# Kernel optimization log

Hardware: AMD Instinct MI355X
Metric: run time of the kernel (lower is better)

The kernel has to match this reference:

```python
import jax, jax.numpy as jnp
import numpy as np

N = 100_000   # nodes
E = 1_600_000 # edges
NEG_SLOPE = 0.2

def _glorot(key, shape):
    fan = shape[0] + shape[-1]
    return jax.random.uniform(key, shape, jnp.float32, -1.0, 1.0) * np.sqrt(6.0 / fan)

def setup_inputs() -> dict:
    key = jax.random.key(0)
    ks = jax.random.split(key, 16)
    x = jax.random.normal(ks[0], (N, 2), jnp.float32)
    edge_index = jax.random.randint(ks[1], (2, E), 0, N)
    edge_weights = jax.random.uniform(ks[2], (E,), jnp.float32)
    # GATConv 1: in=2, out=32, heads=4, edge_dim=1 (lin/lin_edge have no bias in PyG)
    W1    = _glorot(ks[3], (2, 128))
    We1   = _glorot(ks[4], (1, 128))
    attS1 = _glorot(ks[5], (4, 32))
    attD1 = _glorot(ks[6], (4, 32))
    attE1 = _glorot(ks[7], (4, 32))
    b1    = jnp.zeros((128,), jnp.float32)
    # GATConv 2: in=128, out=1, heads=1, concat=False
    W2    = _glorot(ks[8], (128, 1))
    We2   = _glorot(ks[9], (1, 1))
    attS2 = _glorot(ks[10], (1, 1))
    attD2 = _glorot(ks[11], (1, 1))
    attE2 = _glorot(ks[12], (1, 1))
    b2    = jnp.zeros((1,), jnp.float32)
    return dict(x=x, edge_index=edge_index, edge_weights=edge_weights,
                W1=W1, attS1=attS1, attD1=attD1, We1=We1, attE1=attE1, b1=b1,
                W2=W2, attS2=attS2, attD2=attD2, We2=We2, attE2=attE2, b2=b2)

def _gat_layer(x, src, dst, eattr, W, We, a_s, a_d, a_e, b, heads, outc, concat):
    n = x.shape[0]
    # add self-loops; fill_value='mean' -> self-loop edge_attr = mean of incoming edge attrs
    cnt = jax.ops.segment_sum(jnp.ones((eattr.shape[0],), eattr.dtype), dst, num_segments=n)
    loop_attr = jax.ops.segment_sum(eattr, dst, num_segments=n) / jnp.maximum(cnt, 1.0)[:, None]
    loop = jnp.arange(n, dtype=src.dtype)
    src = jnp.concatenate([src, loop])
    dst = jnp.concatenate([dst, loop])
    ea = jnp.concatenate([eattr, loop_attr], axis=0)          # [E+N, edge_dim]
    h = (x @ W).reshape(n, heads, outc)                        # [N,H,C]
    a_src = jnp.sum(h * a_s, axis=-1)                          # [N,H]
    a_dst = jnp.sum(h * a_d, axis=-1)                          # [N,H]
    a_edge = jnp.sum((ea @ We).reshape(-1, heads, outc) * a_e, axis=-1)  # [E+N,H]
    logits = jax.nn.leaky_relu(a_src[src] + a_dst[dst] + a_edge, NEG_SLOPE)
    # scatter-softmax grouped by destination node
    m = jax.ops.segment_max(logits, dst, num_segments=n)       # every node has a self-loop
    p = jnp.exp(logits - m[dst])
    s = jax.ops.segment_sum(p, dst, num_segments=n)
    alpha = p / (s[dst] + 1e-16)                               # [E+N,H]
    out = jax.ops.segment_sum(h[src] * alpha[..., None], dst, num_segments=n)  # [N,H,C]
    out = out.reshape(n, heads * outc) if concat else out.mean(axis=1)
    return out + b

def reference(x, edge_index, edge_weights, W1, attS1, attD1, We1, attE1, b1,
              W2, attS2, attD2, We2, attE2, b2):
    src, dst = edge_index[0], edge_index[1]
    ea = edge_weights[:, None]  # edge_dim=1
    h = _gat_layer(x, src, dst, ea, W1, We1, attS1, attD1, attE1, b1, 4, 32, True)
    h = jax.nn.elu(h)
    out = _gat_layer(h, src, dst, ea, W2, We2, attS2, attD2, attE2, b2, 1, 1, False)
    return out.squeeze(-1)  # [N]
```

## Files before the change

kernel.cpp:

```cpp
#include <hip/hip_runtime.h>

#define N_NODES 100000
#define N_EDGES 1600000
#define NQUAD (N_EDGES / 4)
#define NEG_SLOPE 0.2f

#define NBKT 512
#define BDIV 196
#define NUSED 511
#define PB 500
#define QPB (NQUAD / PB)
#define PBS 512
#define BCAP 4096

typedef int   vint4   __attribute__((ext_vector_type(4)));
typedef float vfloat4 __attribute__((ext_vector_type(4)));

__device__ __forceinline__ float leaky(float v) { return v >= 0.f ? v : NEG_SLOPE * v; }

__global__ void __launch_bounds__(256) k_hist(const int* __restrict__ ei,
                                              int* __restrict__ histT) {
    __shared__ int hist[NBKT];
    int tid = threadIdx.x;
    hist[tid] = 0;
    hist[tid + 256] = 0;
    __syncthreads();
    const vint4* dst4 = (const vint4*)(ei + N_EDGES);
    int q0 = blockIdx.x * QPB;
    for (int q = tid; q < QPB; q += 256) {
        vint4 d = __builtin_nontemporal_load(&dst4[q0 + q]);
        atomicAdd(&hist[d.x / BDIV], 1);
        atomicAdd(&hist[d.y / BDIV], 1);
        atomicAdd(&hist[d.z / BDIV], 1);
        atomicAdd(&hist[d.w / BDIV], 1);
    }
    __syncthreads();
    histT[tid * PBS + blockIdx.x] = hist[tid];
    histT[(tid + 256) * PBS + blockIdx.x] = hist[tid + 256];
}

__global__ void __launch_bounds__(512) k_rowscan(const int* __restrict__ histT,
                                                 int* __restrict__ offT,
                                                 int* __restrict__ btot) {
    __shared__ int sm[512];
    int b = blockIdx.x, tid = threadIdx.x;
    int v = (tid < PB) ? histT[b * PBS + tid] : 0;
    sm[tid] = v;
    __syncthreads();
    for (int off = 1; off < 512; off <<= 1) {
        int t = (tid >= off) ? sm[tid - off] : 0;
        __syncthreads();
        sm[tid] += t;
        __syncthreads();
    }
    if (tid < PB) offT[b * PBS + tid] = sm[tid] - v;
    if (tid == 511) btot[b] = sm[511];
}

__global__ void __launch_bounds__(512) k_bprefix(const int* __restrict__ btot,
                                                 int* __restrict__ bbase,
                                                 int* __restrict__ bcnt,
                                                 const float* __restrict__ W1,
                                                 const float* __restrict__ attS1,
                                                 const float* __restrict__ attD1,
                                                 const float* __restrict__ We1,
                                                 const float* __restrict__ attE1,
                                                 float* __restrict__ consts) {
    __shared__ int sm[512];
    int tid = threadIdx.x;
    if (tid < 8) {
        int r = tid >> 2, h = tid & 3;
        float s = 0.f;
        for (int c = 0; c < 32; ++c) s += W1[r * 128 + h * 32 + c] * attS1[h * 32 + c];
        consts[tid] = s;
    } else if (tid < 16) {
        int u = tid - 8, r = u >> 2, h = u & 3;
        float s = 0.f;
        for (int c = 0; c < 32; ++c) s += W1[r * 128 + h * 32 + c] * attD1[h * 32 + c];
        consts[tid] = s;
    } else if (tid < 20) {
        int h = tid - 16;
        float s = 0.f;
        for (int c = 0; c < 32; ++c) s += We1[h * 32 + c] * attE1[h * 32 + c];
        consts[tid] = s;
    }
    int v = btot[tid];
    sm[tid] = v;
    __syncthreads();
    for (int off = 1; off < 512; off <<= 1) {
        int t = (tid >= off) ? sm[tid - off] : 0;
        __syncthreads();
        sm[tid] += t;
        __syncthreads();
    }
    bbase[tid] = sm[tid] - v;
    bcnt[tid] = v;
}

__global__ void __launch_bounds__(512) k_part(const int* __restrict__ ei,
                                              const float* __restrict__ w,
                                              const int* __restrict__ offT,
                                              const int* __restrict__ bbase,
                                              const float* __restrict__ x,
                                              vint4* __restrict__ staging) {
    __shared__ int lcur[NBKT];
    int tid = threadIdx.x;
    lcur[tid] = offT[tid * PBS + blockIdx.x] + bbase[tid];
    __syncthreads();
    const vint4* src4 = (const vint4*)ei;
    const vint4* dst4 = (const vint4*)(ei + N_EDGES);
    const vfloat4* w4 = (const vfloat4*)w;
    int q0 = blockIdx.x * QPB;
    for (int q = tid; q < QPB; q += 512) {
        vint4 s = __builtin_nontemporal_load(&src4[q0 + q]);
        vint4 d = __builtin_nontemporal_load(&dst4[q0 + q]);
        vfloat4 ww = __builtin_nontemporal_load(&w4[q0 + q]);
#pragma unroll
        for (int j = 0; j < 4; ++j) {
            int dd = (j == 0) ? d.x : (j == 1) ? d.y : (j == 2) ? d.z : d.w;
            int ss = (j == 0) ? s.x : (j == 1) ? s.y : (j == 2) ? s.z : s.w;
            float wv = (j == 0) ? ww.x : (j == 1) ? ww.y : (j == 2) ? ww.z : ww.w;
            int b = dd / BDIV;
            int pos = atomicAdd(&lcur[b], 1);
            float2 xs = *(const float2*)(x + 2 * ss);
            vint4 r = {ss | ((dd - b * BDIV) << 17), __float_as_int(wv),
                       __float_as_int(xs.x), __float_as_int(xs.y)};
            staging[pos] = r;
        }
    }
}

__global__ void __launch_bounds__(512) k_bg1(const int* __restrict__ bbase,
                                             const int* __restrict__ bcnt,
                                             const vint4* __restrict__ staging,
                                             int2* __restrict__ csr2,
                                             const float* __restrict__ x,
                                             const float* __restrict__ consts,
                                             const float* __restrict__ W1,
                                             const float* __restrict__ b1,
                                             const float* __restrict__ W2,
                                             int* __restrict__ deg,
                                             int* __restrict__ rowst,
                                             float* __restrict__ h2,
                                             float* __restrict__ la) {
    __shared__ vint4 seg[BCAP];
    __shared__ float sw[BCAP], sx0[BCAP], sx1[BCAP];
    __shared__ int hist[256];
    __shared__ int lcur[BDIV], rowloc[BDIV], degL[BDIV];
    __shared__ float w10[132], w11[132], b1s[132], w2s[132];
    int b = blockIdx.x, tid = threadIdx.x;
    int base = bbase[b];
    int cnt = min(bcnt[b], BCAP);
    if (tid < 256) hist[tid] = 0;
    for (int j = tid; j < 128; j += 512) {
        int jj = (j >> 5) * 33 + (j & 31);
        w10[jj] = W1[j]; w11[jj] = W1[128 + j]; b1s[jj] = b1[j]; w2s[jj] = W2[j];
    }
    __syncthreads();
    for (int i = tid; i < cnt; i += 512) {
        vint4 r = staging[base + i];
        seg[i] = r;
        atomicAdd(&hist[r.x >> 17], 1);
    }
    __syncthreads();
    int v = (tid < 256) ? hist[tid] : 0;
    for (int off = 1; off < 256; off <<= 1) {
        int t = (tid < 256 && tid >= off) ? hist[tid - off] : 0;
        __syncthreads();
        if (tid < 256) hist[tid] += t;
        __syncthreads();
    }
    int n0 = b * BDIV;
    int nnode = min(BDIV, N_NODES - n0);
    if (tid < nnode) {
        deg[n0 + tid] = v;
        rowst[n0 + tid] = base + hist[tid] - v;
        degL[tid] = v;
        rowloc[tid] = hist[tid] - v;
        lcur[tid] = hist[tid] - v;
    }
    __syncthreads();
    for (int i = tid; i < cnt; i += 512) {
        vint4 r = seg[i];
        int dl = r.x >> 17;
        int pos = atomicAdd(&lcur[dl], 1);
        sw[pos] = __int_as_float(r.y);
        sx0[pos] = __int_as_float(r.z);
        sx1[pos] = __int_as_float(r.w);
        csr2[base + pos] = make_int2(r.x & 0x1FFFF, r.y);
    }
    __syncthreads();
    float c[20];
#pragma unroll
    for (int i = 0; i < 20; ++i) c[i] = consts[i];
    int g = tid >> 3, l = tid & 7;
    for (int j = g; j < nnode; j += 64) {
        int n = n0 + j;
        int rsL = rowloc[j], d = degL[j];
        float2 xn = *(const float2*)(x + 2 * n);
        float adv[4];
#pragma unroll
        for (int h = 0; h < 4; ++h) adv[h] = xn.x * c[8 + h] + xn.y * c[12 + h];
        float s[4] = {0, 0, 0, 0}, X0[4] = {0, 0, 0, 0}, X1[4] = {0, 0, 0, 0};
        float wsum = 0.f;
        for (int k = rsL + l; k < rsL + d; k += 8) {
            float wt = sw[k], x0s = sx0[k], x1s = sx1[k];
            wsum += wt;
#pragma unroll
            for (int h = 0; h < 4; ++h) {
                float as = x0s * c[h] + x1s * c[4 + h];
                float p = __expf(leaky(as + adv[h] + wt * c[16 + h]));
                s[h] += p;
                X0[h] += p * x0s;
                X1[h] += p * x1s;
            }
        }
#pragma unroll
        for (int off = 1; off < 8; off <<= 1) {
            wsum += __shfl_xor(wsum, off);
#pragma unroll
            for (int h = 0; h < 4; ++h) {
                s[h]  += __shfl_xor(s[h], off);
                X0[h] += __shfl_xor(X0[h], off);
                X1[h] += __shfl_xor(X1[h], off);
            }
        }
        float lav = wsum / fmaxf((float)d, 1.f);
#pragma unroll
        for (int h = 0; h < 4; ++h) {
            float aso = xn.x * c[h] + xn.y * c[4 + h];
            float p = __expf(leaky(aso + adv[h] + lav * c[16 + h]));
            s[h] += p;
            X0[h] += p * xn.x;
            X1[h] += p * xn.y;
        }
        int hh = l & 3;
        float sh  = (hh == 0) ? s[0]  : (hh == 1) ? s[1]  : (hh == 2) ? s[2]  : s[3];
        float X0h = (hh == 0) ? X0[0] : (hh == 1) ? X0[1] : (hh == 2) ? X0[2] : X0[3];
        float X1h = (hh == 0) ? X1[0] : (hh == 1) ? X1[1] : (hh == 2) ? X1[2] : X1[3];
        float inv = 1.f / (sh + 1e-16f);
        X0h *= inv;
        X1h *= inv;
        float acc = 0.f;
        int basej = hh * 33 + (l >> 2) * 16;
        for (int cc = 0; cc < 16; ++cc) {
            float vv = X0h * w10[basej + cc] + X1h * w11[basej + cc] + b1s[basej + cc];
            float el = vv > 0.f ? vv : __expf(vv) - 1.f;
            acc += el * w2s[basej + cc];
        }
        acc += __shfl_xor(acc, 1);
        acc += __shfl_xor(acc, 2);
        acc += __shfl_xor(acc, 4);
        if (l == 0) {
            h2[n] = acc;
            la[n] = lav;
        }
    }
}

__global__ void __launch_bounds__(256) k_gather2(const int* __restrict__ deg,
                                                 const int* __restrict__ rowst,
                                                 const int2* __restrict__ csr2,
                                                 const float* __restrict__ h2,
                                                 const float* __restrict__ la,
                                                 const float* __restrict__ attS2,
                                                 const float* __restrict__ attD2,
                                                 const float* __restrict__ We2,
                                                 const float* __restrict__ attE2,
                                                 const float* __restrict__ b2,
                                                 float* __restrict__ out) {
    int t = blockIdx.x * blockDim.x + threadIdx.x;
    int n = t >> 3, l = t & 7;
    if (n >= N_NODES) return;
    float aS = attS2[0], aD = attD2[0], cE = We2[0] * attE2[0], bb = b2[0];
    int rs = rowst[n], d = deg[n];
    float hn = h2[n];
    float hnaD = hn * aD;
    float s = 0.f, acc = 0.f;
    for (int k = rs + l; k < rs + d; k += 8) {
        int2 r = csr2[k];
        float hs = h2[r.x];
        float wt = __int_as_float(r.y);
        float p = __expf(leaky(hs * aS + hnaD + wt * cE));
        s += p;
        acc += p * hs;
    }
#pragma unroll
    for (int off = 1; off < 8; off <<= 1) {
        s   += __shfl_xor(s, off);
        acc += __shfl_xor(acc, off);
    }
    float p = __expf(leaky(hn * aS + hnaD + la[n] * cE));
    s += p;
    acc += p * hn;
    if (l == 0) out[n] = acc / (s + 1e-16f) + bb;
}

extern "C" void kernel_launch(void* const* d_in, const int* in_sizes, int n_in,
                              void* d_out, int out_size, void* d_ws, size_t ws_size,
                              hipStream_t stream) {
    const float* x     = (const float*)d_in[0];
    const int*   ei    = (const int*)d_in[1];
    const float* w     = (const float*)d_in[2];
    const float* W1    = (const float*)d_in[3];
    const float* attS1 = (const float*)d_in[4];
    const float* attD1 = (const float*)d_in[5];
    const float* We1   = (const float*)d_in[6];
    const float* attE1 = (const float*)d_in[7];
    const float* b1    = (const float*)d_in[8];
    const float* W2    = (const float*)d_in[9];
    const float* attS2 = (const float*)d_in[10];
    const float* attD2 = (const float*)d_in[11];
    const float* We2   = (const float*)d_in[12];
    const float* attE2 = (const float*)d_in[13];
    const float* b2    = (const float*)d_in[14];
    float* out = (float*)d_out;

    const size_t N = N_NODES;

    int*   histT   = (int*)d_ws;
    int*   offT    = histT + NBKT * PBS;
    int*   btot    = offT + NBKT * PBS;
    int*   bbase   = btot + NBKT;
    int*   bcnt    = bbase + NBKT;
    float* consts  = (float*)(bcnt + NBKT);
    vint4* staging = (vint4*)(consts + 32);
    int2*  csr2    = (int2*)(staging + N_EDGES);
    int*   deg     = (int*)(csr2 + N_EDGES);
    int*   rowst   = deg + N;
    float* h2      = (float*)(rowst + N);
    float* la      = h2 + N;

    k_hist<<<PB, 256, 0, stream>>>(ei, histT);
    k_rowscan<<<NBKT, 512, 0, stream>>>(histT, offT, btot);
    k_bprefix<<<1, 512, 0, stream>>>(btot, bbase, bcnt, W1, attS1, attD1, We1,
                                     attE1, consts);
    k_part<<<PB, 512, 0, stream>>>(ei, w, offT, bbase, x, staging);
    k_bg1<<<NUSED, 512, 0, stream>>>(bbase, bcnt, staging, csr2, x, consts,
                                     W1, b1, W2, deg, rowst, h2, la);
    k_gather2<<<(8 * N_NODES + 255) / 256, 256, 0, stream>>>(deg, rowst, csr2, h2, la,
                                                             attS2, attD2, We2, attE2,
                                                             b2, out);
}
```

Measured before the change: 179.8 us.

## Shrink staging records to 8 bytes and gather x in layer-1 aggregation

The partition kernel no longer gathers source features x into 16-byte staging records; it writes 8-byte (src|local-dst, weight) pairs instead. The bucket kernel drops the three shared-memory per-edge arrays, keeps only an 8-byte segment buffer, and writes csr2 with the local-dst bits left in place. Layer-1 aggregation then reads csr2 from global memory and gathers x[src] per edge, and layer 2 masks off the extra bits. This halves staging traffic and shared-memory use, which may raise occupancy, at the cost of random x gathers and global reads in the aggregation loop.

```diff
diff --git a/kernel.cpp b/kernel.cpp
--- a/kernel.cpp
+++ b/kernel.cpp
@@ -11,9 +11,10 @@
 #define PB 500
 #define QPB (NQUAD / PB)
 #define PBS 512
-#define BCAP 4096
+#define BCAP 3584
 
 typedef int   vint4   __attribute__((ext_vector_type(4)));
+typedef int   vint2   __attribute__((ext_vector_type(2)));
 typedef float vfloat4 __attribute__((ext_vector_type(4)));
 
 __device__ __forceinline__ float leaky(float v) { return v >= 0.f ? v : NEG_SLOPE * v; }
@@ -101,8 +102,7 @@
                                               const float* __restrict__ w,
                                               const int* __restrict__ offT,
                                               const int* __restrict__ bbase,
-                                              const float* __restrict__ x,
-                                              vint4* __restrict__ staging) {
+                                              int2* __restrict__ staging) {
     __shared__ int lcur[NBKT];
     int tid = threadIdx.x;
     lcur[tid] = offT[tid * PBS + blockIdx.x] + bbase[tid];
@@ -122,17 +122,14 @@
             float wv = (j == 0) ? ww.x : (j == 1) ? ww.y : (j == 2) ? ww.z : ww.w;
             int b = dd / BDIV;
             int pos = atomicAdd(&lcur[b], 1);
-            float2 xs = *(const float2*)(x + 2 * ss);
-            vint4 r = {ss | ((dd - b * BDIV) << 17), __float_as_int(wv),
-                       __float_as_int(xs.x), __float_as_int(xs.y)};
-            staging[pos] = r;
+            staging[pos] = make_int2(ss | ((dd - b * BDIV) << 17), __float_as_int(wv));
         }
     }
 }
 
 __global__ void __launch_bounds__(512) k_bg1(const int* __restrict__ bbase,
                                              const int* __restrict__ bcnt,
-                                             const vint4* __restrict__ staging,
+                                             const int2* __restrict__ staging,
                                              int2* __restrict__ csr2,
                                              const float* __restrict__ x,
                                              const float* __restrict__ consts,
@@ -143,8 +140,7 @@
                                              int* __restrict__ rowst,
                                              float* __restrict__ h2,
                                              float* __restrict__ la) {
-    __shared__ vint4 seg[BCAP];
-    __shared__ float sw[BCAP], sx0[BCAP], sx1[BCAP];
+    __shared__ vint2 seg[BCAP];
     __shared__ int hist[256];
     __shared__ int lcur[BDIV], rowloc[BDIV], degL[BDIV];
     __shared__ float w10[132], w11[132], b1s[132], w2s[132];
@@ -157,8 +153,9 @@
         w10[jj] = W1[j]; w11[jj] = W1[128 + j]; b1s[jj] = b1[j]; w2s[jj] = W2[j];
     }
     __syncthreads();
+    const vint2* st2 = (const vint2*)staging;
     for (int i = tid; i < cnt; i += 512) {
-        vint4 r = staging[base + i];
+        vint2 r = st2[base + i];
         seg[i] = r;
         atomicAdd(&hist[r.x >> 17], 1);
     }
@@ -181,13 +178,9 @@
     }
     __syncthreads();
     for (int i = tid; i < cnt; i += 512) {
-        vint4 r = seg[i];
-        int dl = r.x >> 17;
-        int pos = atomicAdd(&lcur[dl], 1);
-        sw[pos] = __int_as_float(r.y);
-        sx0[pos] = __int_as_float(r.z);
-        sx1[pos] = __int_as_float(r.w);
-        csr2[base + pos] = make_int2(r.x & 0x1FFFF, r.y);
+        vint2 r = seg[i];
+        int pos = atomicAdd(&lcur[r.x >> 17], 1);
+        csr2[base + pos] = make_int2(r.x, r.y);
     }
     __syncthreads();
     float c[20];
@@ -196,7 +189,7 @@
     int g = tid >> 3, l = tid & 7;
     for (int j = g; j < nnode; j += 64) {
         int n = n0 + j;
-        int rsL = rowloc[j], d = degL[j];
+        int rsL = base + rowloc[j], d = degL[j];
         float2 xn = *(const float2*)(x + 2 * n);
         float adv[4];
 #pragma unroll
@@ -204,15 +197,17 @@
         float s[4] = {0, 0, 0, 0}, X0[4] = {0, 0, 0, 0}, X1[4] = {0, 0, 0, 0};
         float wsum = 0.f;
         for (int k = rsL + l; k < rsL + d; k += 8) {
-            float wt = sw[k], x0s = sx0[k], x1s = sx1[k];
+            int2 r = csr2[k];
+            float wt = __int_as_float(r.y);
+            float2 xs = *(const float2*)(x + 2 * (r.x & 0x1FFFF));
             wsum += wt;
 #pragma unroll
             for (int h = 0; h < 4; ++h) {
-                float as = x0s * c[h] + x1s * c[4 + h];
+                float as = xs.x * c[h] + xs.y * c[4 + h];
                 float p = __expf(leaky(as + adv[h] + wt * c[16 + h]));
                 s[h] += p;
-                X0[h] += p * x0s;
-                X1[h] += p * x1s;
+                X0[h] += p * xs.x;
+                X1[h] += p * xs.y;
             }
         }
 #pragma unroll
@@ -279,7 +274,7 @@
     float s = 0.f, acc = 0.f;
     for (int k = rs + l; k < rs + d; k += 8) {
         int2 r = csr2[k];
-        float hs = h2[r.x];
+        float hs = h2[r.x & 0x1FFFF];
         float wt = __int_as_float(r.y);
         float p = __expf(leaky(hs * aS + hnaD + wt * cE));
         s += p;
@@ -324,8 +319,8 @@
     int*   bbase   = btot + NBKT;
     int*   bcnt    = bbase + NBKT;
     float* consts  = (float*)(bcnt + NBKT);
-    vint4* staging = (vint4*)(consts + 32);
-    int2*  csr2    = (int2*)(staging + N_EDGES);
+    int2*  staging = (int2*)(consts + 32);
+    int2*  csr2    = staging + N_EDGES;
     int*   deg     = (int*)(csr2 + N_EDGES);
     int*   rowst   = deg + N;
     float* h2      = (float*)(rowst + N);
@@ -335,7 +330,7 @@
     k_rowscan<<<NBKT, 512, 0, stream>>>(histT, offT, btot);
     k_bprefix<<<1, 512, 0, stream>>>(btot, bbase, bcnt, W1, attS1, attD1, We1,
                                      attE1, consts);
-    k_part<<<PB, 512, 0, stream>>>(ei, w, offT, bbase, x, staging);
+    k_part<<<PB, 512, 0, stream>>>(ei, w, offT, bbase, staging);
     k_bg1<<<NUSED, 512, 0, stream>>>(bbase, bcnt, staging, csr2, x, consts,
                                      W1, b1, W2, deg, rowst, h2, la);
     k_gather2<<<(8 * N_NODES + 255) / 256, 256, 0, stream>>>(deg, rowst, csr2, h2, la,
```

After: 165.2 us. 1.09x faster.
